# Optimization experiments

Measured on AMD Instinct MI355X. Metric: run time of the kernel, lower is better.

## Reference

```python
import jax, jax.numpy as jnp
import numpy as np

K = 3          # kernel_size
STRIDE = 2
PAD = K // 2


def setup_inputs() -> dict:
    key = jax.random.key(0)
    k1, k2, k3 = jax.random.split(key, 3)
    B, C, H, W = 8, 64, 256, 256
    x = jax.random.normal(k1, (B, C, H, W), dtype=jnp.float32)
    # conv_sigma: Conv2d(C, C//2, 3, bias=False), kaiming_normal-ish scale
    w_sigma = jax.random.normal(k2, (C // 2, C, 3, 3), dtype=jnp.float32) * (2.0 / (9 * C)) ** 0.5
    # fc: Linear(C//2, 1)
    w_fc = jax.random.normal(k3, (1, C // 2), dtype=jnp.float32) * 0.1
    b_fc = jnp.zeros((1,), dtype=jnp.float32)
    return {"x": x, "w_sigma": w_sigma, "w_fc": w_fc, "b_fc": b_fc}


def _gaussian_kernels(sigma):
    # sigma: [B, 1] -> normalized Gaussian kernels [B, 1, K, K]
    r = jnp.arange(-PAD, PAD + 1, dtype=jnp.float32)
    d = jnp.sqrt(r[:, None] ** 2 + r[None, :] ** 2)          # [K, K] radial distance
    s = jnp.clip(sigma, 1e-4)[:, :, None, None]              # [B, 1, 1, 1]
    g = (1.0 / (jnp.sqrt(2.0 * jnp.pi) * s)) * jnp.exp(-0.5 * (d / s) ** 2)
    return g / jnp.sum(g, axis=(2, 3), keepdims=True)


def reference(x, w_sigma, w_fc, b_fc):
    B = x.shape[0]
    # sigma branch: 3x3 VALID conv -> relu -> global avgpool -> fc -> sigmoid
    h = jax.lax.conv_general_dilated(
        x, w_sigma, (1, 1), 'VALID',
        dimension_numbers=('NCHW', 'OIHW', 'NCHW'))           # [B, C/2, H-2, W-2]
    h = jax.nn.relu(h).mean(axis=(2, 3))                      # [B, C/2]
    sigma = jax.nn.sigmoid(h @ w_fc.T + b_fc)                 # [B, 1]
    kern = _gaussian_kernels(sigma)                           # [B, 1, K, K]
    # per-sample blur: treat C as batch, B as channels, grouped conv groups=B
    xp = jnp.pad(x.transpose(1, 0, 2, 3),
                 ((0, 0), (0, 0), (PAD, PAD), (PAD, PAD)), mode='reflect')
    out = jax.lax.conv_general_dilated(
        xp, kern, (STRIDE, STRIDE), 'VALID',
        dimension_numbers=('NCHW', 'OIHW', 'NCHW'),
        feature_group_count=B)                                # [C, B, H', W']
    return out
```

## Files before the change

### kernel.cpp

```cpp
#include <hip/hip_runtime.h>
#include <math.h>


typedef __attribute__((ext_vector_type(8))) short s8v;
typedef __attribute__((ext_vector_type(4))) float f4v;

static __device__ inline unsigned short f2bf(float f) {
    union { float f; unsigned int u; } v; v.f = f;
    unsigned int u = v.u;
    unsigned int r = u + 0x7FFFu + ((u >> 16) & 1u);
    return (unsigned short)(r >> 16);
}

static __device__ inline unsigned int pk_bf16(float a, float b) {
    unsigned int r;
    asm("v_cvt_pk_bf16_f32 %0, %1, %2" : "=v"(r) : "v"(a), "v"(b));
    return r;
}

__global__ void prep_kernel(const float* __restrict__ w, float* __restrict__ ws) {
    int i = blockIdx.x * blockDim.x + threadIdx.x;
    if (i < 256) ws[i] = 0.f;
    if (i < 9 * 32 * 64) {
        int ic  = i & 63;
        int oc  = (i >> 6) & 31;
        int tap = i >> 11;
        unsigned short* wtb = (unsigned short*)(ws + 512);
        wtb[i] = f2bf(w[oc * 576 + ic * 9 + tap]);
    }
}

__global__ __launch_bounds__(256, 4) void conv_mfma_kernel(
        const float* __restrict__ x, const unsigned short* __restrict__ wtb,
        float* __restrict__ acc_out) {
    __shared__ __align__(16) unsigned char sx[222 * 128];
    __shared__ float sred[4][32];

    const int bx = blockIdx.x, by = blockIdx.y, b = blockIdx.z;
    const int ox0 = bx * 32, oy0 = by * 4;
    const int tid = threadIdx.x;
    const int lane = tid & 63, w = tid >> 6;
    const int m = lane & 15, q = lane >> 4;

    const float* xb = x + (size_t)b * 64 * 65536;
    for (int k = 0; k < 4; ++k) {
        int i = tid + k * 256;
        if (i < 864) {
            int ch = i % 9;
            int t9 = i / 9;
            int yy = t9 % 6;
            int r4 = t9 / 6;
            int y  = oy0 + yy;      if (y  > 255) y  = 255;
            int xc = ox0 + ch * 4;  if (xc > 252) xc = 252;
            const float* src = xb + ((size_t)r4 << 2) * 65536 + y * 256 + xc;
            float4 v0 = *(const float4*)(src);
            float4 v1 = *(const float4*)(src + 65536);
            float4 v2 = *(const float4*)(src + 131072);
            float4 v3 = *(const float4*)(src + 196608);
            const float* a0 = (const float*)&v0;
            const float* a1 = (const float*)&v1;
            const float* a2 = (const float*)&v2;
            const float* a3 = (const float*)&v3;
            int p0 = yy * 37 + ch * 4;
#pragma unroll
            for (int j = 0; j < 4; ++j) {
                int p = p0 + j;
                unsigned int lo = pk_bf16(a0[j], a1[j]);
                unsigned int hi = pk_bf16(a2[j], a3[j]);
                int cw = (r4 >> 1) ^ ((p >> 1) & 7);
                *(uint2*)(sx + p * 128 + cw * 16 + (r4 & 1) * 8) = make_uint2(lo, hi);
            }
        }
    }

    const unsigned short* wB = wtb + m * 64 + q * 8;
    s8v bc0 = *(const s8v*)(wB);
    s8v bc1 = *(const s8v*)(wB + 1024);
    s8v bc2 = *(const s8v*)(wB + 32);
    s8v bc3 = *(const s8v*)(wB + 1024 + 32);

    __syncthreads();

    f4v acc[2][2];
#pragma unroll
    for (int mt = 0; mt < 2; ++mt)
#pragma unroll
        for (int nt = 0; nt < 2; ++nt) acc[mt][nt] = (f4v)0.f;

    int pb[2];
#pragma unroll
    for (int mt = 0; mt < 2; ++mt)
        pb[mt] = w * 37 + mt * 16 + m;

#pragma unroll
    for (int t = 0; t < 9; ++t) {
        const int off = (t / 3) * 37 + (t % 3);
        s8v bn0, bn1, bn2, bn3;
        if (t < 8) {
            const unsigned short* wN = wB + (t + 1) * 2048;
            bn0 = *(const s8v*)(wN);
            bn1 = *(const s8v*)(wN + 1024);
            bn2 = *(const s8v*)(wN + 32);
            bn3 = *(const s8v*)(wN + 1024 + 32);
        }
#pragma unroll
        for (int mt = 0; mt < 2; ++mt) {
            int p  = pb[mt] + off;
            int q0 = q ^ ((p >> 1) & 7);
            s8v afr = *(const s8v*)(sx + p * 128 + q0 * 16);
            acc[mt][0] = __builtin_amdgcn_mfma_f32_16x16x32_bf16(afr, bc0, acc[mt][0], 0, 0, 0);
            acc[mt][1] = __builtin_amdgcn_mfma_f32_16x16x32_bf16(afr, bc1, acc[mt][1], 0, 0, 0);
        }
#pragma unroll
        for (int mt = 0; mt < 2; ++mt) {
            int p  = pb[mt] + off;
            int q1 = (4 + q) ^ ((p >> 1) & 7);
            s8v afr = *(const s8v*)(sx + p * 128 + q1 * 16);
            acc[mt][0] = __builtin_amdgcn_mfma_f32_16x16x32_bf16(afr, bc2, acc[mt][0], 0, 0, 0);
            acc[mt][1] = __builtin_amdgcn_mfma_f32_16x16x32_bf16(afr, bc3, acc[mt][1], 0, 0, 0);
        }
        if (t < 8) { bc0 = bn0; bc1 = bn1; bc2 = bn2; bc3 = bn3; }
    }

    float s0 = 0.f, s1 = 0.f;
    const int oy = oy0 + w;
#pragma unroll
    for (int mt = 0; mt < 2; ++mt) {
        int oxb = ox0 + mt * 16 + q * 4;
#pragma unroll
        for (int reg = 0; reg < 4; ++reg) {
            bool val = (oxb + reg < 254) && (oy < 254);
            if (val) {
                s0 += fmaxf(acc[mt][0][reg], 0.f);
                s1 += fmaxf(acc[mt][1][reg], 0.f);
            }
        }
    }
    s0 += __shfl_xor(s0, 16, 64); s0 += __shfl_xor(s0, 32, 64);
    s1 += __shfl_xor(s1, 16, 64); s1 += __shfl_xor(s1, 32, 64);
    if (lane < 16) { sred[w][lane] = s0; sred[w][16 + lane] = s1; }
    __syncthreads();
    if (tid < 32)
        atomicAdd(&acc_out[b * 32 + tid],
                  sred[0][tid] + sred[1][tid] + sred[2][tid] + sred[3][tid]);
}

__global__ void sigma_kernel(const float* __restrict__ acc, const float* __restrict__ wfc,
                             const float* __restrict__ bfc, float* __restrict__ kout) {
    int t = threadIdx.x;
    int b = t >> 3, j = t & 7;
    float s = 0.f;
#pragma unroll
    for (int i = 0; i < 4; ++i) s += acc[b * 32 + j + i * 8] * wfc[j + i * 8];
    s += __shfl_xor(s, 4, 8);
    s += __shfl_xor(s, 2, 8);
    s += __shfl_xor(s, 1, 8);
    if (j == 0) {
        float z = s * (1.0f / (254.0f * 254.0f)) + bfc[0];
        float sig = 1.0f / (1.0f + __expf(-z));
        float ss = fmaxf(sig, 1e-4f);
        float inv2 = 0.5f / (ss * ss);
        float e1 = __expf(-inv2);
        float e2 = __expf(-2.0f * inv2);
        float inv_norm = 1.0f / (1.0f + 4.0f * e1 + 4.0f * e2);
        kout[b * 4 + 0] = inv_norm;
        kout[b * 4 + 1] = e1 * inv_norm;
        kout[b * 4 + 2] = e2 * inv_norm;
    }
}

__global__ __launch_bounds__(256) void blur_kernel(
        const float* __restrict__ x, const float* __restrict__ kp,
        float* __restrict__ out) {
    const int c = blockIdx.z, b = blockIdx.y;
    const int tid = threadIdx.x;
    const int qx = tid & 31;
    const int oy = blockIdx.x * 8 + (tid >> 5);

    const float kC = kp[b * 4 + 0];
    const float kE = kp[b * 4 + 1];
    const float kD = kp[b * 4 + 2];

    const float* xb = x + ((size_t)(b * 64 + c)) * 65536;

    float o0 = 0.f, o1 = 0.f, o2 = 0.f, o3 = 0.f;
#pragma unroll
    for (int dy = 0; dy < 3; ++dy) {
        int iy = 2 * oy + dy - 1;
        if (iy < 0) iy = 1;
        const float* row = xb + iy * 256;
        const float4 f0 = *(const float4*)(row + 8 * qx);
        const float4 f1 = *(const float4*)(row + 8 * qx + 4);
        float lf = __shfl_up(f1.w, 1, 64);
        const float sm1 = (qx == 0) ? f0.y : lf;
        const float ka = (dy == 1) ? kE : kD;
        const float kb = (dy == 1) ? kC : kE;
        const float kc2 = (dy == 1) ? kE : kD;
        o0 = fmaf(ka, sm1,  fmaf(kb, f0.x, fmaf(kc2, f0.y, o0)));
        o1 = fmaf(ka, f0.y, fmaf(kb, f0.z, fmaf(kc2, f0.w, o1)));
        o2 = fmaf(ka, f0.w, fmaf(kb, f1.x, fmaf(kc2, f1.y, o2)));
        o3 = fmaf(ka, f1.y, fmaf(kb, f1.z, fmaf(kc2, f1.w, o3)));
    }
    *(float4*)(out + (((size_t)c * 8 + b) * 128 + oy) * 128 + 4 * qx) =
        make_float4(o0, o1, o2, o3);
}

extern "C" void kernel_launch(void* const* d_in, const int* in_sizes, int n_in,
                              void* d_out, int out_size, void* d_ws, size_t ws_size,
                              hipStream_t stream) {
    const float* x       = (const float*)d_in[0];
    const float* w_sigma = (const float*)d_in[1];
    const float* w_fc    = (const float*)d_in[2];
    const float* b_fc    = (const float*)d_in[3];
    float* out = (float*)d_out;
    float* ws  = (float*)d_ws;
    const unsigned short* wtb = (const unsigned short*)(ws + 512);

    prep_kernel<<<72, 256, 0, stream>>>(w_sigma, ws);
    conv_mfma_kernel<<<dim3(8, 64, 8), 256, 0, stream>>>(x, wtb, ws);
    sigma_kernel<<<1, 64, 0, stream>>>(ws, w_fc, b_fc, ws + 256);
    blur_kernel<<<dim3(16, 8, 64), 256, 0, stream>>>(x, ws + 256, out);
}
```

Before: 282.6 us.

## Double-buffer conv input staging across four row tiles per block

Each conv block now handles four consecutive 4-row output tiles instead of one. It stages the next tile's bf16-converted input into a second LDS buffer while computing MFMAs on the current one, and the grid shrinks by four in y. The goal is to hide global-load latency behind compute and cut the block count and the number of atomic adds. In exchange, LDS use doubles, launch bounds drop to 2 blocks per SM, and each tile adds a barrier, which may lower occupancy.

Measured after the change: 291.6 us. 1.03x slower.

```diff
diff --git a/kernel.cpp b/kernel.cpp
--- a/kernel.cpp
+++ b/kernel.cpp
@@ -30,47 +30,62 @@
     }
 }
 
-__global__ __launch_bounds__(256, 4) void conv_mfma_kernel(
+__global__ __launch_bounds__(256, 2) void conv_mfma_kernel(
         const float* __restrict__ x, const unsigned short* __restrict__ wtb,
         float* __restrict__ acc_out) {
-    __shared__ __align__(16) unsigned char sx[222 * 128];
+    __shared__ __align__(16) unsigned char sx[2][222 * 128];
     __shared__ float sred[4][32];
 
-    const int bx = blockIdx.x, by = blockIdx.y, b = blockIdx.z;
-    const int ox0 = bx * 32, oy0 = by * 4;
+    const int bx = blockIdx.x, byg = blockIdx.y, b = blockIdx.z;
+    const int ox0 = bx * 32;
     const int tid = threadIdx.x;
     const int lane = tid & 63, w = tid >> 6;
     const int m = lane & 15, q = lane >> 4;
-
     const float* xb = x + (size_t)b * 64 * 65536;
+
+    int xc_[4], yy_[4], p0_[4], r4_[4];
+    bool vld_[4];
+#pragma unroll
     for (int k = 0; k < 4; ++k) {
-        int i = tid + k * 256;
-        if (i < 864) {
-            int ch = i % 9;
-            int t9 = i / 9;
-            int yy = t9 % 6;
-            int r4 = t9 / 6;
-            int y  = oy0 + yy;      if (y  > 255) y  = 255;
-            int xc = ox0 + ch * 4;  if (xc > 252) xc = 252;
-            const float* src = xb + ((size_t)r4 << 2) * 65536 + y * 256 + xc;
-            float4 v0 = *(const float4*)(src);
-            float4 v1 = *(const float4*)(src + 65536);
-            float4 v2 = *(const float4*)(src + 131072);
-            float4 v3 = *(const float4*)(src + 196608);
-            const float* a0 = (const float*)&v0;
-            const float* a1 = (const float*)&v1;
-            const float* a2 = (const float*)&v2;
-            const float* a3 = (const float*)&v3;
-            int p0 = yy * 37 + ch * 4;
-#pragma unroll
-            for (int j = 0; j < 4; ++j) {
-                int p = p0 + j;
-                unsigned int lo = pk_bf16(a0[j], a1[j]);
-                unsigned int hi = pk_bf16(a2[j], a3[j]);
-                int cw = (r4 >> 1) ^ ((p >> 1) & 7);
-                *(uint2*)(sx + p * 128 + cw * 16 + (r4 & 1) * 8) = make_uint2(lo, hi);
-            }
-        }
+        int i  = tid + k * 256;
+        int ch = i % 9;
+        int t9 = i / 9;
+        yy_[k] = t9 % 6;
+        r4_[k] = (t9 / 6) & 15;
+        int xc = ox0 + ch * 4;  if (xc > 252) xc = 252;
+        xc_[k] = xc;
+        p0_[k] = yy_[k] * 37 + ch * 4;
+        vld_[k] = (i < 864);
+    }
+
+#define STAGE(dst, OY0)                                                        \
+    {                                                                          \
+        _Pragma("unroll")                                                      \
+        for (int k = 0; k < 4; ++k) {                                          \
+            if (vld_[k]) {                                                     \
+                int y = (OY0) + yy_[k];  if (y > 255) y = 255;                 \
+                const float* src = xb + ((size_t)r4_[k] << 2) * 65536          \
+                                      + y * 256 + xc_[k];                      \
+                float4 v0 = *(const float4*)(src);                             \
+                float4 v1 = *(const float4*)(src + 65536);                     \
+                float4 v2 = *(const float4*)(src + 131072);                    \
+                float4 v3 = *(const float4*)(src + 196608);                    \
+                const float* a0 = (const float*)&v0;                           \
+                const float* a1 = (const float*)&v1;                           \
+                const float* a2 = (const float*)&v2;                           \
+                const float* a3 = (const float*)&v3;                           \
+                int r4 = r4_[k];                                               \
+                _Pragma("unroll")                                              \
+                for (int j = 0; j < 4; ++j) {                                  \
+                    int p = p0_[k] + j;                                        \
+                    unsigned int lo = pk_bf16(a0[j], a1[j]);                   \
+                    unsigned int hi = pk_bf16(a2[j], a3[j]);                   \
+                    int cw = (r4 >> 1) ^ ((p >> 1) & 7);                       \
+                    *(uint2*)((dst) + p * 128 + cw * 16 + (r4 & 1) * 8) =      \
+                        make_uint2(lo, hi);                                    \
+                }                                                              \
+            }                                                                  \
+        }                                                                      \
     }
 
     const unsigned short* wB = wtb + m * 64 + q * 8;
@@ -79,63 +94,75 @@
     s8v bc2 = *(const s8v*)(wB + 32);
     s8v bc3 = *(const s8v*)(wB + 1024 + 32);
 
+    STAGE(sx[0], byg * 16)
     __syncthreads();
-
-    f4v acc[2][2];
-#pragma unroll
-    for (int mt = 0; mt < 2; ++mt)
-#pragma unroll
-        for (int nt = 0; nt < 2; ++nt) acc[mt][nt] = (f4v)0.f;
 
     int pb[2];
 #pragma unroll
     for (int mt = 0; mt < 2; ++mt)
         pb[mt] = w * 37 + mt * 16 + m;
 
-#pragma unroll
-    for (int t = 0; t < 9; ++t) {
-        const int off = (t / 3) * 37 + (t % 3);
-        s8v bn0, bn1, bn2, bn3;
-        if (t < 8) {
-            const unsigned short* wN = wB + (t + 1) * 2048;
-            bn0 = *(const s8v*)(wN);
-            bn1 = *(const s8v*)(wN + 1024);
-            bn2 = *(const s8v*)(wN + 32);
-            bn3 = *(const s8v*)(wN + 1024 + 32);
+    float s0 = 0.f, s1 = 0.f;
+
+#pragma unroll
+    for (int t = 0; t < 4; ++t) {
+        const int oy0 = byg * 16 + t * 4;
+        unsigned char* cur = sx[t & 1];
+        unsigned char* alt = sx[(t & 1) ^ 1];
+
+        if (t < 3) STAGE(alt, oy0 + 4)
+
+        f4v acc[2][2];
+#pragma unroll
+        for (int mt = 0; mt < 2; ++mt)
+#pragma unroll
+            for (int nt = 0; nt < 2; ++nt) acc[mt][nt] = (f4v)0.f;
+
+#pragma unroll
+        for (int tp = 0; tp < 9; ++tp) {
+            const int off = (tp / 3) * 37 + (tp % 3);
+            const unsigned short* wN = wB + ((tp + 1) % 9) * 2048;
+            s8v bn0 = *(const s8v*)(wN);
+            s8v bn1 = *(const s8v*)(wN + 1024);
+            s8v bn2 = *(const s8v*)(wN + 32);
+            s8v bn3 = *(const s8v*)(wN + 1024 + 32);
+#pragma unroll
+            for (int mt = 0; mt < 2; ++mt) {
+                int p  = pb[mt] + off;
+                int q0 = q ^ ((p >> 1) & 7);
+                s8v afr = *(const s8v*)(cur + p * 128 + q0 * 16);
+                acc[mt][0] = __builtin_amdgcn_mfma_f32_16x16x32_bf16(afr, bc0, acc[mt][0], 0, 0, 0);
+                acc[mt][1] = __builtin_amdgcn_mfma_f32_16x16x32_bf16(afr, bc1, acc[mt][1], 0, 0, 0);
+            }
+#pragma unroll
+            for (int mt = 0; mt < 2; ++mt) {
+                int p  = pb[mt] + off;
+                int q1 = (4 + q) ^ ((p >> 1) & 7);
+                s8v afr = *(const s8v*)(cur + p * 128 + q1 * 16);
+                acc[mt][0] = __builtin_amdgcn_mfma_f32_16x16x32_bf16(afr, bc2, acc[mt][0], 0, 0, 0);
+                acc[mt][1] = __builtin_amdgcn_mfma_f32_16x16x32_bf16(afr, bc3, acc[mt][1], 0, 0, 0);
+            }
+            bc0 = bn0; bc1 = bn1; bc2 = bn2; bc3 = bn3;
         }
+
+        const int oy = oy0 + w;
 #pragma unroll
         for (int mt = 0; mt < 2; ++mt) {
-            int p  = pb[mt] + off;
-            int q0 = q ^ ((p >> 1) & 7);
-            s8v afr = *(const s8v*)(sx + p * 128 + q0 * 16);
-            acc[mt][0] = __builtin_amdgcn_mfma_f32_16x16x32_bf16(afr, bc0, acc[mt][0], 0, 0, 0);
-            acc[mt][1] = __builtin_amdgcn_mfma_f32_16x16x32_bf16(afr, bc1, acc[mt][1], 0, 0, 0);
-        }
-#pragma unroll
-        for (int mt = 0; mt < 2; ++mt) {
-            int p  = pb[mt] + off;
-            int q1 = (4 + q) ^ ((p >> 1) & 7);
-            s8v afr = *(const s8v*)(sx + p * 128 + q1 * 16);
-            acc[mt][0] = __builtin_amdgcn_mfma_f32_16x16x32_bf16(afr, bc2, acc[mt][0], 0, 0, 0);
-            acc[mt][1] = __builtin_amdgcn_mfma_f32_16x16x32_bf16(afr, bc3, acc[mt][1], 0, 0, 0);
-        }
-        if (t < 8) { bc0 = bn0; bc1 = bn1; bc2 = bn2; bc3 = bn3; }
-    }
-
-    float s0 = 0.f, s1 = 0.f;
-    const int oy = oy0 + w;
-#pragma unroll
-    for (int mt = 0; mt < 2; ++mt) {
-        int oxb = ox0 + mt * 16 + q * 4;
-#pragma unroll
-        for (int reg = 0; reg < 4; ++reg) {
-            bool val = (oxb + reg < 254) && (oy < 254);
-            if (val) {
-                s0 += fmaxf(acc[mt][0][reg], 0.f);
-                s1 += fmaxf(acc[mt][1][reg], 0.f);
+            int oxb = ox0 + mt * 16 + q * 4;
+#pragma unroll
+            for (int reg = 0; reg < 4; ++reg) {
+                bool val = (oxb + reg < 254) && (oy < 254);
+                if (val) {
+                    s0 += fmaxf(acc[mt][0][reg], 0.f);
+                    s1 += fmaxf(acc[mt][1][reg], 0.f);
+                }
             }
         }
-    }
+
+        __syncthreads();
+    }
+#undef STAGE
+
     s0 += __shfl_xor(s0, 16, 64); s0 += __shfl_xor(s0, 32, 64);
     s1 += __shfl_xor(s1, 16, 64); s1 += __shfl_xor(s1, 32, 64);
     if (lane < 16) { sred[w][lane] = s0; sred[w][16 + lane] = s1; }
@@ -217,7 +244,7 @@
     const unsigned short* wtb = (const unsigned short*)(ws + 512);
 
     prep_kernel<<<72, 256, 0, stream>>>(w_sigma, ws);
-    conv_mfma_kernel<<<dim3(8, 64, 8), 256, 0, stream>>>(x, wtb, ws);
+    conv_mfma_kernel<<<dim3(8, 16, 8), 256, 0, stream>>>(x, wtb, ws);
     sigma_kernel<<<1, 64, 0, stream>>>(ws, w_fc, b_fc, ws + 256);
     blur_kernel<<<dim3(16, 8, 64), 256, 0, stream>>>(x, ws + 256, out);
 }
```
